# Kernel optimization log

Measured on AMD Instinct MI355X. Metric: run time of the kernel, lower is better.

Reference implementation:

```python
import jax, jax.numpy as jnp
import numpy as np

TOPK = 32

def setup_inputs() -> dict:
    key = jax.random.key(0)
    k1, k2, k3, k4 = jax.random.split(key, 4)
    x = jax.random.normal(k1, (8, 1024, 1024), dtype=jnp.float32)
    values = jax.random.normal(k2, (262144, 512), dtype=jnp.float32) * 0.01
    keys1 = jax.random.normal(k3, (512, 512), dtype=jnp.float32) * 0.01
    keys2 = jax.random.normal(k4, (512, 512), dtype=jnp.float32) * 0.01
    return {"x": x, "values": values, "keys1": keys1, "keys2": keys2}

def reference(x, values, keys1, keys2):
    D = x.shape[-1]
    n_small = keys1.shape[0]
    # two half-dim key scorings: [..., n_small]
    scores1_full = jnp.einsum('...d,bd->...b', x[..., :D // 2], keys1)
    scores2_full = jnp.einsum('...d,bd->...b', x[..., D // 2:], keys2)
    scores1, indices1 = jax.lax.top_k(scores1_full, TOPK)   # [..., k]
    scores2, indices2 = jax.lax.top_k(scores2_full, TOPK)
    # cartesian product of the two top-k sets: [..., k, k] -> [..., k*k]
    indices12 = indices1[..., :, None] * n_small + indices2[..., None, :]
    scores12 = scores1[..., :, None] * scores2[..., None, :]
    batch_shape = x.shape[:-1]
    scores12 = scores12.reshape(*batch_shape, TOPK * TOPK)
    indices12 = indices12.reshape(*batch_shape, TOPK * TOPK)
    scores, indices = jax.lax.top_k(scores12, TOPK)          # [..., k]
    value_indices = jnp.take_along_axis(indices12, indices, axis=-1)  # [..., k]
    gathered = values[value_indices]                          # [..., k, M]
    y = jnp.einsum('...b,...bm->...m', jax.nn.softmax(scores, axis=-1), gathered)
    return y
```

## Files before the change

### kernel.cpp

```cpp
#include <hip/hip_runtime.h>

#define TOPK 32

__device__ __forceinline__ unsigned monokey(float f) {
  unsigned u = __float_as_uint(f);
  return (u & 0x80000000u) ? ~u : (u | 0x80000000u);
}
__device__ __forceinline__ float inv_monokey(unsigned k) {
  return __uint_as_float((k & 0x80000000u) ? (k ^ 0x80000000u) : ~k);
}
__device__ __forceinline__ void lgkm_fence() {
  asm volatile("s_waitcnt lgkmcnt(0)" ::: "memory");
}

template <int N>
__device__ __forceinline__ unsigned radix_thresh(const unsigned* k) {
  unsigned prefix = 0;
  for (int b = 31; b >= 0; --b) {
    unsigned cand = prefix | (1u << b);
    int c = 0;
#pragma unroll
    for (int j = 0; j < N; ++j)
      c += __popcll(__ballot(k[j] >= cand));
    if (c >= TOPK) {
      prefix = cand;
      if (c == TOPK) break;
    }
  }
  return prefix;
}

__device__ __forceinline__ int lds_off(int r, int g) {
  return r * 32 + ((g ^ ((r >> 3) & 7)) << 2);
}

__global__ __launch_bounds__(256) void score_gemm(
    const float* __restrict__ x,
    const float* __restrict__ keys1,
    const float* __restrict__ keys2,
    float* __restrict__ scores) {
  __shared__ __align__(16) float As[128 * 32];
  __shared__ __align__(16) float Bs[128 * 32];

  const int row0 = blockIdx.x * 128;
  const int col0 = blockIdx.y * 128;

  const float* Kp;
  int xoff, kb;
  if (col0 < 512) { Kp = keys1; xoff = 0;   kb = col0; }
  else            { Kp = keys2; xoff = 512; kb = col0 - 512; }

  const int tid = threadIdx.x;
  const int g = tid & 7;
  const int rb = tid >> 3;
  const int tx = tid & 15, ty = tid >> 4;
  const int m0 = ty * 8, n0 = tx * 8;

  float acc[8][8] = {};

  for (int k0 = 0; k0 < 512; k0 += 32) {
#pragma unroll
    for (int h = 0; h < 4; ++h) {
      const int r = rb + h * 32;
      float4 av = *(const float4*)&x[(size_t)(row0 + r) * 1024 + xoff + k0 + g * 4];
      *(float4*)&As[lds_off(r, g)] = av;
      float4 bv = *(const float4*)&Kp[(size_t)(kb + r) * 512 + k0 + g * 4];
      *(float4*)&Bs[lds_off(r, g)] = bv;
    }
    __syncthreads();

#pragma unroll
    for (int G = 0; G < 8; ++G) {
      float4 a[8], b[8];
#pragma unroll
      for (int i = 0; i < 8; ++i) a[i] = *(const float4*)&As[lds_off(m0 + i, G)];
#pragma unroll
      for (int j = 0; j < 8; ++j) b[j] = *(const float4*)&Bs[lds_off(n0 + j, G)];
#pragma unroll
      for (int i = 0; i < 8; ++i)
#pragma unroll
        for (int j = 0; j < 8; ++j) {
          acc[i][j] = fmaf(a[i].x, b[j].x, acc[i][j]);
          acc[i][j] = fmaf(a[i].y, b[j].y, acc[i][j]);
          acc[i][j] = fmaf(a[i].z, b[j].z, acc[i][j]);
          acc[i][j] = fmaf(a[i].w, b[j].w, acc[i][j]);
        }
    }
    __syncthreads();
  }

#pragma unroll
  for (int i = 0; i < 8; ++i) {
    float4 o0 = {acc[i][0], acc[i][1], acc[i][2], acc[i][3]};
    float4 o1 = {acc[i][4], acc[i][5], acc[i][6], acc[i][7]};
    float* dst = &scores[(size_t)(row0 + m0 + i) * 1024 + col0 + n0];
    *(float4*)&dst[0] = o0;
    *(float4*)&dst[4] = o1;
  }
}

__global__ __launch_bounds__(256) void topk_gather(
    const float* __restrict__ scores,
    const float* __restrict__ values,
    float* __restrict__ y) {
  const int wid = threadIdx.x >> 6;
  const int lane = threadIdx.x & 63;
  const int row = blockIdx.x * 4 + wid;
  const float* srow = scores + (size_t)row * 1024;

  unsigned k1[8], k2[8];
  {
    float4 a = *(const float4*)&srow[4 * lane];
    float4 b = *(const float4*)&srow[256 + 4 * lane];
    k1[0] = monokey(a.x); k1[1] = monokey(a.y); k1[2] = monokey(a.z); k1[3] = monokey(a.w);
    k1[4] = monokey(b.x); k1[5] = monokey(b.y); k1[6] = monokey(b.z); k1[7] = monokey(b.w);
    float4 c = *(const float4*)&srow[512 + 4 * lane];
    float4 d = *(const float4*)&srow[768 + 4 * lane];
    k2[0] = monokey(c.x); k2[1] = monokey(c.y); k2[2] = monokey(c.z); k2[3] = monokey(c.w);
    k2[4] = monokey(d.x); k2[5] = monokey(d.y); k2[6] = monokey(d.z); k2[7] = monokey(d.w);
  }

  __shared__ float s1v[4][TOPK], s2v[4][TOPK], tvv[4][TOPK], wts[4][TOPK];
  __shared__ int s1i[4][TOPK], s2i[4][TOPK], vidx[4][TOPK];

  const unsigned long long mlt = (1ull << lane) - 1;

  {
    unsigned T = radix_thresh<8>(k1);
    int base = 0;
#pragma unroll
    for (int j = 0; j < 8; ++j) {
      bool take = (k1[j] >= T);
      unsigned long long m = __ballot(take);
      int pos = base + __popcll(m & mlt);
      if (take && pos < TOPK) {
        s1v[wid][pos] = inv_monokey(k1[j]);
        s1i[wid][pos] = (j < 4) ? 4 * lane + j : 256 + 4 * lane + (j - 4);
      }
      base += __popcll(m);
    }
  }
  {
    unsigned T = radix_thresh<8>(k2);
    int base = 0;
#pragma unroll
    for (int j = 0; j < 8; ++j) {
      bool take = (k2[j] >= T);
      unsigned long long m = __ballot(take);
      int pos = base + __popcll(m & mlt);
      if (take && pos < TOPK) {
        s2v[wid][pos] = inv_monokey(k2[j]);
        s2i[wid][pos] = (j < 4) ? 4 * lane + j : 256 + 4 * lane + (j - 4);
      }
      base += __popcll(m);
    }
  }
  lgkm_fence();

  {
    const int r1 = lane >> 1;
    const int j0 = (lane & 1) * 16;
    const float a1 = s1v[wid][r1];
    unsigned kp[16];
#pragma unroll
    for (int j = 0; j < 16; ++j) kp[j] = monokey(a1 * s2v[wid][j0 + j]);

    unsigned T = radix_thresh<16>(kp);
    int base = 0;
#pragma unroll
    for (int j = 0; j < 16; ++j) {
      bool take = (kp[j] >= T);
      unsigned long long m = __ballot(take);
      int pos = base + __popcll(m & mlt);
      if (take && pos < TOPK) {
        int lin = 16 * lane + j;
        tvv[wid][pos] = inv_monokey(kp[j]);
        vidx[wid][pos] = s1i[wid][lin >> 5] * 512 + s2i[wid][lin & 31];
      }
      base += __popcll(m);
    }
  }
  lgkm_fence();

  {
    float v = (lane < TOPK) ? tvv[wid][lane] : -__builtin_inff();
    float mx = v;
#pragma unroll
    for (int off = 32; off; off >>= 1) mx = fmaxf(mx, __shfl_xor(mx, off));
    float e = (lane < TOPK) ? __expf(v - mx) : 0.0f;
    float s = e;
#pragma unroll
    for (int off = 32; off; off >>= 1) s += __shfl_xor(s, off);
    if (lane < TOPK) wts[wid][lane] = e / s;
  }
  lgkm_fence();

  float4 acc0 = {0, 0, 0, 0}, acc1 = {0, 0, 0, 0};
  for (int t0 = 0; t0 < TOPK; t0 += 8) {
    float w[8];
    const float* vr[8];
#pragma unroll
    for (int u = 0; u < 8; ++u) {
      w[u] = wts[wid][t0 + u];
      vr[u] = values + (size_t)vidx[wid][t0 + u] * 512;
    }
    float4 va[8], vb[8];
#pragma unroll
    for (int u = 0; u < 8; ++u) {
      va[u] = *(const float4*)&vr[u][4 * lane];
      vb[u] = *(const float4*)&vr[u][256 + 4 * lane];
    }
#pragma unroll
    for (int u = 0; u < 8; ++u) {
      acc0.x = fmaf(w[u], va[u].x, acc0.x);
      acc0.y = fmaf(w[u], va[u].y, acc0.y);
      acc0.z = fmaf(w[u], va[u].z, acc0.z);
      acc0.w = fmaf(w[u], va[u].w, acc0.w);
      acc1.x = fmaf(w[u], vb[u].x, acc1.x);
      acc1.y = fmaf(w[u], vb[u].y, acc1.y);
      acc1.z = fmaf(w[u], vb[u].z, acc1.z);
      acc1.w = fmaf(w[u], vb[u].w, acc1.w);
    }
  }
  float* yr = y + (size_t)row * 512;
  *(float4*)&yr[4 * lane] = acc0;
  *(float4*)&yr[256 + 4 * lane] = acc1;
}

extern "C" void kernel_launch(void* const* d_in, const int* in_sizes, int n_in,
                              void* d_out, int out_size, void* d_ws, size_t ws_size,
                              hipStream_t stream) {
  const float* x      = (const float*)d_in[0];
  const float* values = (const float*)d_in[1];
  const float* keys1  = (const float*)d_in[2];
  const float* keys2  = (const float*)d_in[3];
  float* y = (float*)d_out;

  const int R = in_sizes[0] / 1024;
  float* scores = (float*)d_ws;

  dim3 gridA(R / 128, 8);
  score_gemm<<<gridA, 256, 0, stream>>>(x, keys1, keys2, scores);
  topk_gather<<<R / 4, 256, 0, stream>>>(scores, values, y);
}
```

Before: 215.3 us.

## Double-buffer score GEMM tiles with direct global-to-LDS async loads

Replaces the register-staged global-to-shared copies in the score GEMM with direct global_load_lds transfers of 16 bytes per lane. The A and B tiles are now double-buffered so the next k-step's load is issued before the current tile is computed. The XOR swizzle is applied on the global address side, so the LDS read pattern stays the same. This aims to hide global memory latency and free registers, at the cost of twice the LDS footprint and reliance on the compiler placing the right vmcnt waits before the barrier.

```diff
diff --git a/kernel.cpp b/kernel.cpp
--- a/kernel.cpp
+++ b/kernel.cpp
@@ -34,13 +34,21 @@
   return r * 32 + ((g ^ ((r >> 3) & 7)) << 2);
 }
 
+__device__ __forceinline__ void gl_lds16f(const float* g, float* l) {
+  __builtin_amdgcn_global_load_lds(
+      (const __attribute__((address_space(1))) unsigned int*)g,
+      (__attribute__((address_space(3))) unsigned int*)l, 16, 0, 0);
+}
+
+#define NSTEPA 16
+
 __global__ __launch_bounds__(256) void score_gemm(
     const float* __restrict__ x,
     const float* __restrict__ keys1,
     const float* __restrict__ keys2,
     float* __restrict__ scores) {
-  __shared__ __align__(16) float As[128 * 32];
-  __shared__ __align__(16) float Bs[128 * 32];
+  __shared__ __align__(16) float As[2][128 * 32];
+  __shared__ __align__(16) float Bs[2][128 * 32];
 
   const int row0 = blockIdx.x * 128;
   const int col0 = blockIdx.y * 128;
@@ -51,31 +59,40 @@
   else            { Kp = keys2; xoff = 512; kb = col0 - 512; }
 
   const int tid = threadIdx.x;
-  const int g = tid & 7;
-  const int rb = tid >> 3;
+  const int w = tid >> 6;
+  const int lane = tid & 63;
+  const int grow = lane >> 3;
   const int tx = tid & 15, ty = tid >> 4;
   const int m0 = ty * 8, n0 = tx * 8;
 
   float acc[8][8] = {};
 
-  for (int k0 = 0; k0 < 512; k0 += 32) {
-#pragma unroll
-    for (int h = 0; h < 4; ++h) {
-      const int r = rb + h * 32;
-      float4 av = *(const float4*)&x[(size_t)(row0 + r) * 1024 + xoff + k0 + g * 4];
-      *(float4*)&As[lds_off(r, g)] = av;
-      float4 bv = *(const float4*)&Kp[(size_t)(kb + r) * 512 + k0 + g * 4];
-      *(float4*)&Bs[lds_off(r, g)] = bv;
-    }
-    __syncthreads();
+#define STAGEA(buf, t)                                                              \
+  {                                                                                 \
+    _Pragma("unroll") for (int i = 0; i < 4; ++i) {                                 \
+      int r = 32 * w + 8 * i;                                                       \
+      int gslot = (lane & 7) ^ ((r >> 3) & 7);                                      \
+      gl_lds16f(&x[(size_t)(row0 + r + grow) * 1024 + xoff + (t)*32 + gslot * 4],   \
+                &As[buf][r * 32]);                                                  \
+      gl_lds16f(&Kp[(size_t)(kb + r + grow) * 512 + (t)*32 + gslot * 4],            \
+                &Bs[buf][r * 32]);                                                  \
+    }                                                                               \
+  }
+
+  STAGEA(0, 0);
+  __syncthreads();
+
+  int cur = 0;
+  for (int t = 0; t < NSTEPA; ++t) {
+    if (t + 1 < NSTEPA) STAGEA(cur ^ 1, t + 1);
 
 #pragma unroll
     for (int G = 0; G < 8; ++G) {
       float4 a[8], b[8];
 #pragma unroll
-      for (int i = 0; i < 8; ++i) a[i] = *(const float4*)&As[lds_off(m0 + i, G)];
-#pragma unroll
-      for (int j = 0; j < 8; ++j) b[j] = *(const float4*)&Bs[lds_off(n0 + j, G)];
+      for (int i = 0; i < 8; ++i) a[i] = *(const float4*)&As[cur][lds_off(m0 + i, G)];
+#pragma unroll
+      for (int j = 0; j < 8; ++j) b[j] = *(const float4*)&Bs[cur][lds_off(n0 + j, G)];
 #pragma unroll
       for (int i = 0; i < 8; ++i)
 #pragma unroll
@@ -87,6 +104,7 @@
         }
     }
     __syncthreads();
+    cur ^= 1;
   }
 
 #pragma unroll
```

New measurement: 243.8 us. 13.2% more time.
